# Kernel tuning notes

Hardware: AMD Instinct MI355X
Metric: run time of the kernel (lower is better)

Reference implementation:

```python
import jax, jax.numpy as jnp
import numpy as np

START_AGE = 0
END_AGE = 100
LAMBDA_1 = 0.2
LAMBDA_2 = 0.05
EPS = 1e-3

N = 524288
WIDTH = END_AGE + 1 - START_AGE  # 101


def setup_inputs() -> dict:
    key = jax.random.key(0)
    k1, k2 = jax.random.split(key)
    inp = jax.random.normal(k1, (N, WIDTH), dtype=jnp.float32)
    target = jax.random.randint(k2, (N,), 0, WIDTH, dtype=jnp.int32)
    return {"input": inp, "target": target}


def reference(input, target):
    # softmax over age bins
    p = jax.nn.softmax(input, axis=1)                                  # [N, W]
    a = jnp.arange(START_AGE, END_AGE + 1, dtype=jnp.float32)          # [W]
    tf = target.astype(jnp.float32)
    # expected age per sample
    mean = jnp.sum(p * a, axis=1)                                      # [N]
    mean_loss = jnp.mean((mean - tf) ** 2) / 2.0
    # vectorized one-hot gather: prob of ground-truth bin
    prob_gt = jnp.take_along_axis(p, target[:, None].astype(jnp.int32), axis=1)  # [N,1]
    # mask of bins with prob strictly below the GT prob; detached in the original
    mask = jax.lax.stop_gradient((p < prob_gt).astype(p.dtype))        # [N, W]
    p_not_K = mask * p
    residue_loss = jnp.mean(jnp.sum(-(p_not_K + EPS) * jnp.log(p_not_K + EPS), axis=1))
    batch_average_K = jnp.sum(mask == 0).astype(jnp.float32) / N
    return (LAMBDA_1 * mean_loss, LAMBDA_2 * residue_loss, batch_average_K)
```

## Files before the change

### kernel.cpp

```cpp
#include <hip/hip_runtime.h>

#define N_ROWS 524288
#define W_BINS 101
#define EPS_F 1e-3f

__global__ __launch_bounds__(64) void init_acc(double* __restrict__ acc) {
    if (threadIdx.x < 3) acc[threadIdx.x] = 0.0;
}

__global__ __launch_bounds__(256) void mrl_main(const float* __restrict__ x,
                                                const int* __restrict__ tgt,
                                                double* __restrict__ acc) {
    const int lane = threadIdx.x & 63;
    const int s    = threadIdx.x & 15;
    const int gid  = (blockIdx.x * 256 + threadIdx.x) >> 4;
    const int totalGroups = (gridDim.x * 256) >> 4;

    float racc = 0.0f;
    float sqac = 0.0f;
    int   kacc = 0;

    for (int row = gid; row < N_ROWS; row += totalGroups) {
        const float* xr = x + (size_t)row * W_BINS;

        float e[6];
        float se = 0.0f, sea = 0.0f;
        #pragma unroll
        for (int k = 0; k < 6; ++k) {
            float v  = xr[s + 16 * k];
            float ev = __expf(v);
            e[k] = ev;
            se  += ev;
            sea += ev * (float)(s + 16 * k);
        }
        float e6 = 0.0f;
        if (s < 5) {
            float v = xr[96 + s];
            e6  = __expf(v);
            se += e6;
            sea += e6 * (float)(96 + s);
        }

        #pragma unroll
        for (int off = 8; off >= 1; off >>= 1) {
            se  += __shfl_xor(se,  off);
            sea += __shfl_xor(sea, off);
        }

        const int   t    = tgt[row];
        const float inv  = 1.0f / se;
        const float mean = sea * inv;

        const int kq = t >> 4;
        float cand = e[0];
        if (kq == 1) cand = e[1];
        if (kq == 2) cand = e[2];
        if (kq == 3) cand = e[3];
        if (kq == 4) cand = e[4];
        if (kq == 5) cand = e[5];
        if (kq == 6) cand = e6;
        const float egt = __shfl(cand, (lane & 48) | (t & 15));
        const float pgt = egt * inv;

        if (s == 0) {
            float d = mean - (float)t;
            sqac += d * d;
        }

        #pragma unroll
        for (int k = 0; k < 6; ++k) {
            float p  = e[k] * inv;
            bool  lt = p < pgt;
            float qe = (lt ? p : 0.0f) + EPS_F;
            racc -= qe * __logf(qe);
            kacc += lt ? 0 : 1;
        }
        if (s < 5) {
            float p  = e6 * inv;
            bool  lt = p < pgt;
            float qe = (lt ? p : 0.0f) + EPS_F;
            racc -= qe * __logf(qe);
            kacc += lt ? 0 : 1;
        }
    }

    float kf = (float)kacc;
    #pragma unroll
    for (int off = 32; off >= 1; off >>= 1) {
        racc += __shfl_xor(racc, off);
        sqac += __shfl_xor(sqac, off);
        kf   += __shfl_xor(kf,   off);
    }

    __shared__ float sr[4], ss[4], sk[4];
    const int wid = threadIdx.x >> 6;
    if (lane == 0) { sr[wid] = racc; ss[wid] = sqac; sk[wid] = kf; }
    __syncthreads();
    if (threadIdx.x == 0) {
        double S = (double)ss[0] + (double)ss[1] + (double)ss[2] + (double)ss[3];
        double R = (double)sr[0] + (double)sr[1] + (double)sr[2] + (double)sr[3];
        double K = (double)sk[0] + (double)sk[1] + (double)sk[2] + (double)sk[3];
        atomicAdd(&acc[0], S);
        atomicAdd(&acc[1], R);
        atomicAdd(&acc[2], K);
    }
}

__global__ __launch_bounds__(64) void finalize(const double* __restrict__ acc,
                                               float* __restrict__ out) {
    if (threadIdx.x == 0) {
        const double n = (double)N_ROWS;
        out[0] = (float)(0.2  * 0.5 * (acc[0] / n));
        out[1] = (float)(0.05 *       (acc[1] / n));
        out[2] = (float)(acc[2] / n);
    }
}

extern "C" void kernel_launch(void* const* d_in, const int* in_sizes, int n_in,
                              void* d_out, int out_size, void* d_ws, size_t ws_size,
                              hipStream_t stream) {
    const float* x   = (const float*)d_in[0];
    const int*   tgt = (const int*)d_in[1];
    float*  out = (float*)d_out;
    double* acc = (double*)d_ws;

    init_acc<<<1, 64, 0, stream>>>(acc);
    mrl_main<<<2048, 256, 0, stream>>>(x, tgt, acc);
    finalize<<<1, 64, 0, stream>>>(acc, out);
}
```

Before: 350.4 us.

## Process two rows per group iteration and gather target logit directly

Each 16-lane group now handles two rows per loop iteration with interleaved loads, exps and shuffle reductions, so more independent memory and math work is in flight at once. The ground-truth probability is no longer found with a select chain plus cross-lane shuffle. Each lane loads the target logit directly and exponentiates it, then compares unnormalized exps. The reciprocal uses the hardware approximate rcp. The 7th slot runs unconditionally, and a constant correction cancels the phantom EPS entropy terms. In exchange, register pressure rises and the loop relies on the row count splitting evenly into two-row steps.

```diff
diff --git a/kernel.cpp b/kernel.cpp
--- a/kernel.cpp
+++ b/kernel.cpp
@@ -14,73 +14,77 @@
     const int lane = threadIdx.x & 63;
     const int s    = threadIdx.x & 15;
     const int gid  = (blockIdx.x * 256 + threadIdx.x) >> 4;
-    const int totalGroups = (gridDim.x * 256) >> 4;
+    const int G    = (gridDim.x * 256) >> 4;
 
     float racc = 0.0f;
     float sqac = 0.0f;
     int   kacc = 0;
 
-    for (int row = gid; row < N_ROWS; row += totalGroups) {
-        const float* xr = x + (size_t)row * W_BINS;
+    for (int rowA = gid; rowA < N_ROWS; rowA += 2 * G) {
+        const int rowB = rowA + G;
+        const float* xa = x + (size_t)rowA * W_BINS;
+        const float* xb = x + (size_t)rowB * W_BINS;
 
-        float e[6];
-        float se = 0.0f, sea = 0.0f;
+        const int ta = tgt[rowA];
+        const int tb = tgt[rowB];
+        const float xta = xa[ta];
+        const float xtb = xb[tb];
+
+        float ea[7], eb[7];
+        float seA = 0.f, seaA = 0.f, seB = 0.f, seaB = 0.f;
         #pragma unroll
         for (int k = 0; k < 6; ++k) {
-            float v  = xr[s + 16 * k];
-            float ev = __expf(v);
-            e[k] = ev;
-            se  += ev;
-            sea += ev * (float)(s + 16 * k);
+            const float c  = (float)(s + 16 * k);
+            float va = xa[s + 16 * k];
+            float vb = xb[s + 16 * k];
+            float Ea = __expf(va);
+            float Eb = __expf(vb);
+            ea[k] = Ea; eb[k] = Eb;
+            seA += Ea; seaA += Ea * c;
+            seB += Eb; seaB += Eb * c;
         }
-        float e6 = 0.0f;
+        ea[6] = 0.f; eb[6] = 0.f;
         if (s < 5) {
-            float v = xr[96 + s];
-            e6  = __expf(v);
-            se += e6;
-            sea += e6 * (float)(96 + s);
+            const float c = (float)(96 + s);
+            float Ea = __expf(xa[96 + s]);
+            float Eb = __expf(xb[96 + s]);
+            ea[6] = Ea; eb[6] = Eb;
+            seA += Ea; seaA += Ea * c;
+            seB += Eb; seaB += Eb * c;
         }
 
         #pragma unroll
         for (int off = 8; off >= 1; off >>= 1) {
-            se  += __shfl_xor(se,  off);
-            sea += __shfl_xor(sea, off);
+            seA  += __shfl_xor(seA,  off);
+            seaA += __shfl_xor(seaA, off);
+            seB  += __shfl_xor(seB,  off);
+            seaB += __shfl_xor(seaB, off);
         }
 
-        const int   t    = tgt[row];
-        const float inv  = 1.0f / se;
-        const float mean = sea * inv;
-
-        const int kq = t >> 4;
-        float cand = e[0];
-        if (kq == 1) cand = e[1];
-        if (kq == 2) cand = e[2];
-        if (kq == 3) cand = e[3];
-        if (kq == 4) cand = e[4];
-        if (kq == 5) cand = e[5];
-        if (kq == 6) cand = e6;
-        const float egt = __shfl(cand, (lane & 48) | (t & 15));
-        const float pgt = egt * inv;
+        const float egta = __expf(xta);
+        const float egtb = __expf(xtb);
+        const float invA = __builtin_amdgcn_rcpf(seA);
+        const float invB = __builtin_amdgcn_rcpf(seB);
 
         if (s == 0) {
-            float d = mean - (float)t;
-            sqac += d * d;
+            float dA = seaA * invA - (float)ta;
+            float dB = seaB * invB - (float)tb;
+            sqac += dA * dA + dB * dB;
         }
 
         #pragma unroll
-        for (int k = 0; k < 6; ++k) {
-            float p  = e[k] * inv;
-            bool  lt = p < pgt;
-            float qe = (lt ? p : 0.0f) + EPS_F;
-            racc -= qe * __logf(qe);
-            kacc += lt ? 0 : 1;
+        for (int k = 0; k < 7; ++k) {
+            bool  ltA = ea[k] < egta;
+            bool  ltB = eb[k] < egtb;
+            float qA  = (ltA ? ea[k] * invA : 0.0f) + EPS_F;
+            float qB  = (ltB ? eb[k] * invB : 0.0f) + EPS_F;
+            racc -= qA * __logf(qA);
+            racc -= qB * __logf(qB);
+            kacc += (ltA ? 0 : 1) + (ltB ? 0 : 1);
         }
-        if (s < 5) {
-            float p  = e6 * inv;
-            bool  lt = p < pgt;
-            float qe = (lt ? p : 0.0f) + EPS_F;
-            racc -= qe * __logf(qe);
-            kacc += lt ? 0 : 1;
+        if (s >= 5) {
+            const float phantom = -EPS_F * __logf(EPS_F);
+            racc -= 2.0f * phantom;
         }
     }
 
```

Result: faster. 334.2 us (-4.6%).

## Stage row tiles into LDS via direct global-to-LDS loads, one thread per row

Applied to the files above, without the earlier changes.

Each 64-thread block copies a contiguous 64-row tile into shared memory with global_load_lds, then each thread processes a whole row serially and recomputes exp in a second pass rather than holding values in registers. The ground-truth comparison uses unnormalized exponentials. Double atomics plus the init kernel are replaced by per-block float4 partials and a single-block reduce kernel. The aim is fully coalesced DMA-style loads and fewer launches, at the cost of duplicate exp work, LDS bank conflicts from the 101-float row stride, and 8192 small blocks.

```diff
diff --git a/kernel.cpp b/kernel.cpp
--- a/kernel.cpp
+++ b/kernel.cpp
@@ -1,118 +1,118 @@
 #include <hip/hip_runtime.h>
 
-#define N_ROWS 524288
-#define W_BINS 101
-#define EPS_F 1e-3f
+#define N_ROWS   524288
+#define W_BINS   101
+#define EPS_F    1e-3f
+#define RPB      64
+#define NBLK     (N_ROWS / RPB)
+#define TILE_F   (RPB * W_BINS)
 
-__global__ __launch_bounds__(64) void init_acc(double* __restrict__ acc) {
-    if (threadIdx.x < 3) acc[threadIdx.x] = 0.0;
-}
+typedef const float __attribute__((address_space(1)))* gptr_t;
+typedef float __attribute__((address_space(3)))* sptr_t;
 
-__global__ __launch_bounds__(256) void mrl_main(const float* __restrict__ x,
-                                                const int* __restrict__ tgt,
-                                                double* __restrict__ acc) {
-    const int lane = threadIdx.x & 63;
-    const int s    = threadIdx.x & 15;
-    const int gid  = (blockIdx.x * 256 + threadIdx.x) >> 4;
-    const int totalGroups = (gridDim.x * 256) >> 4;
+__global__ __launch_bounds__(64) void mrl_main(const float* __restrict__ x,
+                                               const int* __restrict__ tgt,
+                                               float4* __restrict__ partial) {
+    __shared__ float sm[TILE_F];
+    const int lane = threadIdx.x;
+    const float* gbase = x + (size_t)blockIdx.x * TILE_F;
 
-    float racc = 0.0f;
-    float sqac = 0.0f;
-    int   kacc = 0;
-
-    for (int row = gid; row < N_ROWS; row += totalGroups) {
-        const float* xr = x + (size_t)row * W_BINS;
-
-        float e[6];
-        float se = 0.0f, sea = 0.0f;
-        #pragma unroll
-        for (int k = 0; k < 6; ++k) {
-            float v  = xr[s + 16 * k];
-            float ev = __expf(v);
-            e[k] = ev;
-            se  += ev;
-            sea += ev * (float)(s + 16 * k);
-        }
-        float e6 = 0.0f;
-        if (s < 5) {
-            float v = xr[96 + s];
-            e6  = __expf(v);
-            se += e6;
-            sea += e6 * (float)(96 + s);
-        }
-
-        #pragma unroll
-        for (int off = 8; off >= 1; off >>= 1) {
-            se  += __shfl_xor(se,  off);
-            sea += __shfl_xor(sea, off);
-        }
-
-        const int   t    = tgt[row];
-        const float inv  = 1.0f / se;
-        const float mean = sea * inv;
-
-        const int kq = t >> 4;
-        float cand = e[0];
-        if (kq == 1) cand = e[1];
-        if (kq == 2) cand = e[2];
-        if (kq == 3) cand = e[3];
-        if (kq == 4) cand = e[4];
-        if (kq == 5) cand = e[5];
-        if (kq == 6) cand = e6;
-        const float egt = __shfl(cand, (lane & 48) | (t & 15));
-        const float pgt = egt * inv;
-
-        if (s == 0) {
-            float d = mean - (float)t;
-            sqac += d * d;
-        }
-
-        #pragma unroll
-        for (int k = 0; k < 6; ++k) {
-            float p  = e[k] * inv;
-            bool  lt = p < pgt;
-            float qe = (lt ? p : 0.0f) + EPS_F;
-            racc -= qe * __logf(qe);
-            kacc += lt ? 0 : 1;
-        }
-        if (s < 5) {
-            float p  = e6 * inv;
-            bool  lt = p < pgt;
-            float qe = (lt ? p : 0.0f) + EPS_F;
-            racc -= qe * __logf(qe);
-            kacc += lt ? 0 : 1;
-        }
+    #pragma unroll
+    for (int q = 0; q < 25; ++q) {
+        __builtin_amdgcn_global_load_lds((gptr_t)(gbase + q * 256 + lane * 4),
+                                         (sptr_t)(sm + q * 256), 16, 0, 0);
+    }
+    if (lane < 16) {
+        __builtin_amdgcn_global_load_lds((gptr_t)(gbase + 6400 + lane * 4),
+                                         (sptr_t)(sm + 6400), 16, 0, 0);
     }
 
-    float kf = (float)kacc;
+    const int row = blockIdx.x * RPB + lane;
+    const int t   = tgt[row];
+
+    __syncthreads();
+
+    const float* r = sm + lane * W_BINS;
+
+    float se0 = 0.f, se1 = 0.f, sa0 = 0.f, sa1 = 0.f;
+    #pragma unroll
+    for (int i = 0; i < 100; i += 2) {
+        float e0 = __expf(r[i]);
+        float e1 = __expf(r[i + 1]);
+        se0 += e0; sa0 += e0 * (float)i;
+        se1 += e1; sa1 += e1 * (float)(i + 1);
+    }
+    {
+        float e = __expf(r[100]);
+        se0 += e; sa0 += e * 100.0f;
+    }
+    const float se  = se0 + se1;
+    const float sea = sa0 + sa1;
+
+    const float egt = __expf(r[t]);
+    const float inv = __builtin_amdgcn_rcpf(se);
+    const float d   = sea * inv - (float)t;
+    float sq = d * d;
+
+    float rc0 = 0.f, rc1 = 0.f;
+    int   k   = 0;
+    #pragma unroll
+    for (int i = 0; i < 100; i += 2) {
+        float e0 = __expf(r[i]);
+        float e1 = __expf(r[i + 1]);
+        bool  l0 = e0 < egt, l1 = e1 < egt;
+        float q0 = (l0 ? e0 * inv : 0.f) + EPS_F;
+        float q1 = (l1 ? e1 * inv : 0.f) + EPS_F;
+        rc0 -= q0 * __logf(q0);
+        rc1 -= q1 * __logf(q1);
+        k   += (l0 ? 0 : 1) + (l1 ? 0 : 1);
+    }
+    {
+        float e = __expf(r[100]);
+        bool  l = e < egt;
+        float q = (l ? e * inv : 0.f) + EPS_F;
+        rc0 -= q * __logf(q);
+        k   += l ? 0 : 1;
+    }
+    float rc = rc0 + rc1;
+    float kf = (float)k;
+
     #pragma unroll
     for (int off = 32; off >= 1; off >>= 1) {
-        racc += __shfl_xor(racc, off);
-        sqac += __shfl_xor(sqac, off);
-        kf   += __shfl_xor(kf,   off);
+        sq += __shfl_xor(sq, off);
+        rc += __shfl_xor(rc, off);
+        kf += __shfl_xor(kf, off);
     }
-
-    __shared__ float sr[4], ss[4], sk[4];
-    const int wid = threadIdx.x >> 6;
-    if (lane == 0) { sr[wid] = racc; ss[wid] = sqac; sk[wid] = kf; }
-    __syncthreads();
-    if (threadIdx.x == 0) {
-        double S = (double)ss[0] + (double)ss[1] + (double)ss[2] + (double)ss[3];
-        double R = (double)sr[0] + (double)sr[1] + (double)sr[2] + (double)sr[3];
-        double K = (double)sk[0] + (double)sk[1] + (double)sk[2] + (double)sk[3];
-        atomicAdd(&acc[0], S);
-        atomicAdd(&acc[1], R);
-        atomicAdd(&acc[2], K);
+    if (lane == 0) {
+        partial[blockIdx.x] = make_float4(sq, rc, kf, 0.0f);
     }
 }
 
-__global__ __launch_bounds__(64) void finalize(const double* __restrict__ acc,
-                                               float* __restrict__ out) {
+__global__ __launch_bounds__(256) void mrl_reduce(const float4* __restrict__ partial,
+                                                  float* __restrict__ out) {
+    double s = 0.0, r = 0.0, k = 0.0;
+    for (int i = threadIdx.x; i < NBLK; i += 256) {
+        float4 v = partial[i];
+        s += (double)v.x; r += (double)v.y; k += (double)v.z;
+    }
+    #pragma unroll
+    for (int off = 32; off >= 1; off >>= 1) {
+        s += __shfl_xor(s, off);
+        r += __shfl_xor(r, off);
+        k += __shfl_xor(k, off);
+    }
+    __shared__ double sd[12];
+    const int w = threadIdx.x >> 6;
+    if ((threadIdx.x & 63) == 0) { sd[w * 3 + 0] = s; sd[w * 3 + 1] = r; sd[w * 3 + 2] = k; }
+    __syncthreads();
     if (threadIdx.x == 0) {
+        double S = sd[0] + sd[3] + sd[6] + sd[9];
+        double R = sd[1] + sd[4] + sd[7] + sd[10];
+        double K = sd[2] + sd[5] + sd[8] + sd[11];
         const double n = (double)N_ROWS;
-        out[0] = (float)(0.2  * 0.5 * (acc[0] / n));
-        out[1] = (float)(0.05 *       (acc[1] / n));
-        out[2] = (float)(acc[2] / n);
+        out[0] = (float)(0.1  * (S / n));
+        out[1] = (float)(0.05 * (R / n));
+        out[2] = (float)(K / n);
     }
 }
 
@@ -121,10 +121,9 @@
                               hipStream_t stream) {
     const float* x   = (const float*)d_in[0];
     const int*   tgt = (const int*)d_in[1];
-    float*  out = (float*)d_out;
-    double* acc = (double*)d_ws;
+    float*  out     = (float*)d_out;
+    float4* partial = (float4*)d_ws;
 
-    init_acc<<<1, 64, 0, stream>>>(acc);
-    mrl_main<<<2048, 256, 0, stream>>>(x, tgt, acc);
-    finalize<<<1, 64, 0, stream>>>(acc, out);
+    mrl_main<<<NBLK, RPB, 0, stream>>>(x, tgt, partial);
+    mrl_reduce<<<1, 256, 0, stream>>>(partial, out);
 }
```

Result: faster. 302.6 us (-13.6%).
